# Performance work log

Measured on AMD Instinct MI355X. Metric: run time of the kernel, lower is better.

Reference implementation:

```python
import jax, jax.numpy as jnp
import numpy as np

N_NODES = 50000

def _sage_conv(x, src, dst, W_l, b_l, W_r):
    # PyG SAGEConv, aggr='mean': out = lin_l(mean_j x_j) + lin_r(x_i)
    msg = x[src]                                                 # [E, d] gather
    agg = jax.ops.segment_sum(msg, dst, num_segments=N_NODES)   # [N, d] scatter-add
    cnt = jax.ops.segment_sum(jnp.ones((src.shape[0], 1), x.dtype), dst,
                              num_segments=N_NODES)              # [N, 1] in-degree
    agg = agg / jnp.maximum(cnt, 1.0)                            # mean (0 for isolated nodes)
    return agg @ W_l + b_l + x @ W_r

def setup_inputs() -> dict:
    key = jax.random.key(0)
    ks = jax.random.split(key, 8)
    in_f, hid, out_f = 128, 128, 64
    E = 640000
    x = jax.random.normal(ks[0], (N_NODES, in_f), dtype=jnp.float32)
    edge_index = jax.random.randint(ks[1], (2, E), 0, N_NODES, dtype=jnp.int64)
    def glorot(k, fan_in, fan_out):
        lim = (6.0 / (fan_in + fan_out)) ** 0.5
        return jax.random.uniform(k, (fan_in, fan_out), jnp.float32, -lim, lim)
    return {
        "x": x,
        "edge_index": edge_index,
        "W1_l": glorot(ks[2], in_f, hid),
        "b1": jnp.zeros((hid,), jnp.float32),
        "W1_r": glorot(ks[3], in_f, hid),
        "W2_l": glorot(ks[4], hid, out_f),
        "b2": jnp.zeros((out_f,), jnp.float32),
        "W2_r": glorot(ks[5], hid, out_f),
    }

def reference(x, edge_index, W1_l, b1, W1_r, W2_l, b2, W2_r):
    src, dst = edge_index[0], edge_index[1]
    h = _sage_conv(x, src, dst, W1_l, b1, W1_r)
    h = jax.nn.relu(h)
    # dropout: eval mode -> identity (deterministic reference)
    h = _sage_conv(h, src, dst, W2_l, b2, W2_r)
    return h
```

## Files before the change

### kernel.cpp

```cpp
#include <hip/hip_runtime.h>
#include <cstddef>

static constexpr int N_NODES = 50000;
static constexpr int E_EDGES = 640000;
static constexpr int F = 128;
static constexpr int MAXD = 64;
static constexpr int NBINS = 196;
static constexpr int BINCAP = 4096;
static constexpr int EBLK  = 250;

typedef __bf16 b8 __attribute__((ext_vector_type(8)));
typedef float  f4 __attribute__((ext_vector_type(4)));
typedef float  f2 __attribute__((ext_vector_type(2)));

__device__ inline unsigned short f2bf(float f) {
    unsigned u = __float_as_uint(f);
    u += 0x7FFF + ((u >> 16) & 1);
    return (unsigned short)(u >> 16);
}

__device__ inline void accq(float* s, uint2 u) {
    f2 p;
    p = __builtin_amdgcn_cvt_pk_f32_fp8(u.x, false); s[0] += p.x; s[1] += p.y;
    p = __builtin_amdgcn_cvt_pk_f32_fp8(u.x, true);  s[2] += p.x; s[3] += p.y;
    p = __builtin_amdgcn_cvt_pk_f32_fp8(u.y, false); s[4] += p.x; s[5] += p.y;
    p = __builtin_amdgcn_cvt_pk_f32_fp8(u.y, true);  s[6] += p.x; s[7] += p.y;
}

template<int BN>
__device__ inline void pack_w_body(int t, const float* __restrict__ Wl,
                                   const float* __restrict__ Wr, uint4* __restrict__ Bp) {
    constexpr int NTg = BN / 16;
    int wid = t >> 6, lane = t & 63;
    if (wid >= 8 * NTg) return;
    int kq = lane >> 4, m = lane & 15;
    int kt = wid / NTg, nt = wid % NTg;
    unsigned short tmp[8];
#pragma unroll
    for (int j = 0; j < 8; ++j) {
        int k = kt * 32 + kq * 8 + j;
        const float* W = (k < 128) ? Wl : Wr;
        tmp[j] = f2bf(W[(size_t)(k & 127) * BN + nt * 16 + m]);
    }
    uint4 u;
    u.x = tmp[0] | ((unsigned)tmp[1] << 16);
    u.y = tmp[2] | ((unsigned)tmp[3] << 16);
    u.z = tmp[4] | ((unsigned)tmp[5] << 16);
    u.w = tmp[6] | ((unsigned)tmp[7] << 16);
    Bp[wid * 64 + lane] = u;
}

__global__ __launch_bounds__(256)
void prep(const int* __restrict__ ei, int* __restrict__ gbin, unsigned* __restrict__ binbuf,
          const float* __restrict__ x, uint4* __restrict__ xb, uint2* __restrict__ xq,
          const float* __restrict__ W1l, const float* __restrict__ W1r, uint4* __restrict__ Bp1,
          const float* __restrict__ W2l, const float* __restrict__ W2r, uint4* __restrict__ Bp2) {
    int b = blockIdx.x, tid = threadIdx.x;
    if (b < EBLK) {
        __shared__ int cnt[NBINS];
        __shared__ int base[NBINS];
        for (int i = tid; i < NBINS; i += 256) cnt[i] = 0;
        __syncthreads();
        int e0 = b * 2560;
        unsigned rec[10]; int bin[10]; int rnk[10];
#pragma unroll
        for (int k = 0; k < 10; ++k) {
            int e = e0 + k * 256 + tid;
            int s = ei[e], d = ei[E_EDGES + e];
            bin[k] = d >> 8;
            rec[k] = ((unsigned)(d & 255) << 16) | (unsigned)s;
            rnk[k] = atomicAdd(&cnt[bin[k]], 1);
        }
        __syncthreads();
        for (int i = tid; i < NBINS; i += 256)
            base[i] = atomicAdd(&gbin[i], cnt[i]);
        __syncthreads();
#pragma unroll
        for (int k = 0; k < 10; ++k) {
            int pos = base[bin[k]] + rnk[k];
            if (pos < BINCAP) binbuf[(size_t)bin[k] * BINCAP + pos] = rec[k];
        }
    } else {
        int o = b - EBLK;
        if (o < 3125) {
            int i = o * 256 + tid;
            const float4* s = (const float4*)x + (size_t)i * 2;
            float4 v0 = s[0], v1 = s[1];
            uint4 u;
            u.x = f2bf(v0.x) | ((unsigned)f2bf(v0.y) << 16);
            u.y = f2bf(v0.z) | ((unsigned)f2bf(v0.w) << 16);
            u.z = f2bf(v1.x) | ((unsigned)f2bf(v1.y) << 16);
            u.w = f2bf(v1.z) | ((unsigned)f2bf(v1.w) << 16);
            xb[i] = u;
            uint2 q;
            q.x = __builtin_amdgcn_cvt_pk_fp8_f32(v0.x, v0.y, 0, false);
            q.x = __builtin_amdgcn_cvt_pk_fp8_f32(v0.z, v0.w, q.x, true);
            q.y = __builtin_amdgcn_cvt_pk_fp8_f32(v1.x, v1.y, 0, false);
            q.y = __builtin_amdgcn_cvt_pk_fp8_f32(v1.z, v1.w, q.y, true);
            xq[i] = q;
        } else if (o < 3141) {
            pack_w_body<128>((o - 3125) * 256 + tid, W1l, W1r, Bp1);
        } else {
            pack_w_body<64>((o - 3141) * 256 + tid, W2l, W2r, Bp2);
        }
    }
}

__global__ __launch_bounds__(256)
void bucket(const unsigned* __restrict__ binbuf, const int* __restrict__ gbin,
            int* __restrict__ deg, int* __restrict__ col) {
    int b = blockIdx.x, tid = threadIdx.x;
    __shared__ int lc[256];
    lc[tid] = 0;
    __syncthreads();
    int cnt = gbin[b]; cnt = cnt < BINCAP ? cnt : BINCAP;
    const unsigned* bb = binbuf + (size_t)b * BINCAP;
    for (int i = tid; i < cnt; i += 256) {
        unsigned rec = bb[i];
        int dl = (rec >> 16) & 255;
        int s  = (int)(rec & 0xFFFFu);
        int r  = atomicAdd(&lc[dl], 1);
        if (r < MAXD) col[(((size_t)(b << 8) + dl) << 6) + r] = s;
    }
    __syncthreads();
    int node = (b << 8) + tid;
    if (node < N_NODES) deg[node] = lc[tid];
}

__global__ __launch_bounds__(256)
void sage_l1(const uint2* __restrict__ featq,
             const unsigned short* __restrict__ featb,
             const int* __restrict__ deg,
             const int* __restrict__ col,
             const unsigned short* __restrict__ Bp1,
             const unsigned short* __restrict__ Bp2,
             const float* __restrict__ b1,
             const float* __restrict__ b2,
             unsigned char* __restrict__ Zq,
             float* __restrict__ out) {
    constexpr int LDW = 68;
    __shared__ unsigned Alds[16 * LDW];
    __shared__ unsigned short Hlds[16 * 136];

    const int tid  = threadIdx.x;
    const int wv   = tid >> 6;
    const int lane = tid & 63;
    const int c    = lane & 15;
    const int g    = lane >> 4;
    const int node0 = blockIdx.x * 16;
    const int node  = node0 + wv * 4 + g;

    {
        int d0 = deg[node];
        int d  = d0 < MAXD ? d0 : MAXD;
        int jb = node << 6, je = jb + d;
        float s0[8] = {0.f,0.f,0.f,0.f,0.f,0.f,0.f,0.f};
        float s1[8] = {0.f,0.f,0.f,0.f,0.f,0.f,0.f,0.f};
        float s2[8] = {0.f,0.f,0.f,0.f,0.f,0.f,0.f,0.f};
        float s3[8] = {0.f,0.f,0.f,0.f,0.f,0.f,0.f,0.f};
        int j = jb;
        for (; j + 7 < je; j += 8) {
            uint2 u0 = featq[(size_t)col[j + 0] * 16 + c];
            uint2 u1 = featq[(size_t)col[j + 1] * 16 + c];
            uint2 u2 = featq[(size_t)col[j + 2] * 16 + c];
            uint2 u3 = featq[(size_t)col[j + 3] * 16 + c];
            uint2 u4 = featq[(size_t)col[j + 4] * 16 + c];
            uint2 u5 = featq[(size_t)col[j + 5] * 16 + c];
            uint2 u6 = featq[(size_t)col[j + 6] * 16 + c];
            uint2 u7 = featq[(size_t)col[j + 7] * 16 + c];
            accq(s0, u0); accq(s1, u1); accq(s2, u2); accq(s3, u3);
            accq(s0, u4); accq(s1, u5); accq(s2, u6); accq(s3, u7);
        }
        if (j + 3 < je) {
            uint2 u0 = featq[(size_t)col[j + 0] * 16 + c];
            uint2 u1 = featq[(size_t)col[j + 1] * 16 + c];
            uint2 u2 = featq[(size_t)col[j + 2] * 16 + c];
            uint2 u3 = featq[(size_t)col[j + 3] * 16 + c];
            accq(s0, u0); accq(s1, u1); accq(s2, u2); accq(s3, u3);
            j += 4;
        }
        for (; j < je; ++j) {
            uint2 u0 = featq[(size_t)col[j] * 16 + c];
            accq(s0, u0);
        }
        float inv = 1.0f / (float)(d > 0 ? d : 1);
        float r[8];
#pragma unroll
        for (int k = 0; k < 8; ++k) r[k] = ((s0[k] + s1[k]) + (s2[k] + s3[k])) * inv;
        uint4 o;
        o.x = f2bf(r[0]) | ((unsigned)f2bf(r[1]) << 16);
        o.y = f2bf(r[2]) | ((unsigned)f2bf(r[3]) << 16);
        o.z = f2bf(r[4]) | ((unsigned)f2bf(r[5]) << 16);
        o.w = f2bf(r[6]) | ((unsigned)f2bf(r[7]) << 16);
        *((uint4*)&Alds[(wv * 4 + g) * LDW + c * 4]) = o;
    }
    __syncthreads();

    const int m  = lane & 15;
    const int kq = lane >> 4;
    const unsigned short* srow = featb + (size_t)(node0 + m) * F + kq * 8;

    f4 zero = {0.f, 0.f, 0.f, 0.f};
    f4 acc[2] = {zero, zero};
#pragma unroll
    for (int kt = 0; kt < 8; ++kt) {
        b8 a;
        if (kt < 4) a = *((const b8*)((const char*)Alds + m * 272 + kt * 64 + kq * 16));
        else        a = *((const b8*)(srow + (kt - 4) * 32));
#pragma unroll
        for (int t = 0; t < 2; ++t) {
            int nt = wv * 2 + t;
            b8 b = *((const b8*)(Bp1 + ((size_t)(kt * 8 + nt) * 64 + lane) * 8));
            acc[t] = __builtin_amdgcn_mfma_f32_16x16x32_bf16(a, b, acc[t], 0, 0, 0);
        }
    }
    {
        int rowb = kq * 4;
#pragma unroll
        for (int t = 0; t < 2; ++t) {
            int cc = (wv * 2 + t) * 16 + m;
            float bv = b1[cc];
#pragma unroll
            for (int r = 0; r < 4; ++r) {
                float v = fmaxf(acc[t][r] + bv, 0.0f);
                Hlds[(rowb + r) * 136 + cc] = f2bf(v);
            }
        }
    }
    __syncthreads();

    f4 accZ = zero, accS = zero;
#pragma unroll
    for (int kt = 0; kt < 4; ++kt) {
        b8 a = *((const b8*)((const char*)Hlds + m * 272 + kt * 64 + kq * 16));
        b8 bz = *((const b8*)(Bp2 + ((size_t)(kt * 4 + wv) * 64 + lane) * 8));
        b8 bs = *((const b8*)(Bp2 + ((size_t)((kt + 4) * 4 + wv) * 64 + lane) * 8));
        accZ = __builtin_amdgcn_mfma_f32_16x16x32_bf16(a, bz, accZ, 0, 0, 0);
        accS = __builtin_amdgcn_mfma_f32_16x16x32_bf16(a, bs, accS, 0, 0, 0);
    }
    {
        int rowg = node0 + kq * 4;
        int cc = wv * 16 + m;
        float bv = b2[cc];
#pragma unroll
        for (int r = 0; r < 4; ++r) {
            unsigned q = __builtin_amdgcn_cvt_pk_fp8_f32(accZ[r], accZ[r], 0, false);
            Zq[(size_t)(rowg + r) * 64 + cc] = (unsigned char)(q & 0xFF);
            out[(size_t)(rowg + r) * 64 + cc] = accS[r] + bv;
        }
    }
}

__global__ __launch_bounds__(256)
void gather_add(const uint2* __restrict__ Zq,
                const int* __restrict__ deg,
                const int* __restrict__ col,
                float* __restrict__ out, int N) {
    int t = blockIdx.x * 256 + threadIdx.x;
    int node = t >> 3;
    if (node >= N) return;
    int c = t & 7;

    int d0 = deg[node];
    int d  = d0 < MAXD ? d0 : MAXD;
    int jb = node << 6, je = jb + d;
    float s0[8] = {0.f,0.f,0.f,0.f,0.f,0.f,0.f,0.f};
    float s1[8] = {0.f,0.f,0.f,0.f,0.f,0.f,0.f,0.f};
    float s2[8] = {0.f,0.f,0.f,0.f,0.f,0.f,0.f,0.f};
    float s3[8] = {0.f,0.f,0.f,0.f,0.f,0.f,0.f,0.f};
    int j = jb;
    for (; j + 7 < je; j += 8) {
        uint2 u0 = Zq[(size_t)col[j + 0] * 8 + c];
        uint2 u1 = Zq[(size_t)col[j + 1] * 8 + c];
        uint2 u2 = Zq[(size_t)col[j + 2] * 8 + c];
        uint2 u3 = Zq[(size_t)col[j + 3] * 8 + c];
        uint2 u4 = Zq[(size_t)col[j + 4] * 8 + c];
        uint2 u5 = Zq[(size_t)col[j + 5] * 8 + c];
        uint2 u6 = Zq[(size_t)col[j + 6] * 8 + c];
        uint2 u7 = Zq[(size_t)col[j + 7] * 8 + c];
        accq(s0, u0); accq(s1, u1); accq(s2, u2); accq(s3, u3);
        accq(s0, u4); accq(s1, u5); accq(s2, u6); accq(s3, u7);
    }
    if (j + 3 < je) {
        uint2 u0 = Zq[(size_t)col[j + 0] * 8 + c];
        uint2 u1 = Zq[(size_t)col[j + 1] * 8 + c];
        uint2 u2 = Zq[(size_t)col[j + 2] * 8 + c];
        uint2 u3 = Zq[(size_t)col[j + 3] * 8 + c];
        accq(s0, u0); accq(s1, u1); accq(s2, u2); accq(s3, u3);
        j += 4;
    }
    for (; j < je; ++j) {
        uint2 u0 = Zq[(size_t)col[j] * 8 + c];
        accq(s0, u0);
    }
    float inv = 1.0f / (float)(d > 0 ? d : 1);
    float* op = out + (size_t)node * 64 + c * 8;
#pragma unroll
    for (int q = 0; q < 2; ++q) {
        float4 o = *((float4*)(op + q * 4));
        o.x += ((s0[q*4+0] + s1[q*4+0]) + (s2[q*4+0] + s3[q*4+0])) * inv;
        o.y += ((s0[q*4+1] + s1[q*4+1]) + (s2[q*4+1] + s3[q*4+1])) * inv;
        o.z += ((s0[q*4+2] + s1[q*4+2]) + (s2[q*4+2] + s3[q*4+2])) * inv;
        o.w += ((s0[q*4+3] + s1[q*4+3]) + (s2[q*4+3] + s3[q*4+3])) * inv;
        *((float4*)(op + q * 4)) = o;
    }
}


extern "C" void kernel_launch(void* const* d_in, const int* in_sizes, int n_in,
                              void* d_out, int out_size, void* d_ws, size_t ws_size,
                              hipStream_t stream) {
    const float* x   = (const float*)d_in[0];
    const int*   ei  = (const int*)d_in[1];
    const float* W1l = (const float*)d_in[2];
    const float* b1  = (const float*)d_in[3];
    const float* W1r = (const float*)d_in[4];
    const float* W2l = (const float*)d_in[5];
    const float* b2  = (const float*)d_in[6];
    const float* W2r = (const float*)d_in[7];
    float* out = (float*)d_out;

    unsigned* Zq    = (unsigned*)d_ws;
    unsigned* xb    = Zq + (size_t)N_NODES * 16;
    unsigned* xq    = xb + (size_t)N_NODES * 64;
    unsigned* Bp1   = xq + (size_t)N_NODES * 32;
    unsigned* Bp2   = Bp1 + 16384;
    int* col        = (int*)(Bp2 + 8192);
    int* deg        = col + (size_t)N_NODES * MAXD;
    int* gbin       = deg + N_NODES;
    unsigned* binbuf = (unsigned*)(gbin + 256);

    hipMemsetAsync(gbin, 0, 256 * sizeof(int), stream);

    prep<<<EBLK + 3149, 256, 0, stream>>>(ei, gbin, binbuf, x, (uint4*)xb, (uint2*)xq,
                                          W1l, W1r, (uint4*)Bp1, W2l, W2r, (uint4*)Bp2);

    bucket<<<NBINS, 256, 0, stream>>>(binbuf, gbin, deg, col);

    sage_l1<<<N_NODES / 16, 256, 0, stream>>>(
        (const uint2*)xq, (const unsigned short*)xb, deg, col,
        (const unsigned short*)Bp1, (const unsigned short*)Bp2,
        b1, b2, (unsigned char*)Zq, out);

    gather_add<<<(N_NODES * 8 + 255) / 256, 256, 0, stream>>>(
        (const uint2*)Zq, deg, col, out, N_NODES);
}
```

Before: 156.1 us.

## Split neighbor gathers across two lanes per node with shuffle reduction

```diff
diff --git a/kernel.cpp b/kernel.cpp
--- a/kernel.cpp
+++ b/kernel.cpp
@@ -127,7 +127,7 @@
     if (node < N_NODES) deg[node] = lc[tid];
 }
 
-__global__ __launch_bounds__(256)
+__global__ __launch_bounds__(512)
 void sage_l1(const uint2* __restrict__ featq,
              const unsigned short* __restrict__ featb,
              const int* __restrict__ deg,
@@ -145,54 +145,63 @@
     const int tid  = threadIdx.x;
     const int wv   = tid >> 6;
     const int lane = tid & 63;
-    const int c    = lane & 15;
-    const int g    = lane >> 4;
     const int node0 = blockIdx.x * 16;
-    const int node  = node0 + wv * 4 + g;
 
     {
+        const int n  = wv * 2 + (lane >> 5);
+        const int h  = (lane >> 4) & 1;
+        const int c  = lane & 15;
+        const int node = node0 + n;
         int d0 = deg[node];
         int d  = d0 < MAXD ? d0 : MAXD;
-        int jb = node << 6, je = jb + d;
+        int jb = node << 6;
+        int dh = (d + 1 - h) >> 1;
         float s0[8] = {0.f,0.f,0.f,0.f,0.f,0.f,0.f,0.f};
         float s1[8] = {0.f,0.f,0.f,0.f,0.f,0.f,0.f,0.f};
         float s2[8] = {0.f,0.f,0.f,0.f,0.f,0.f,0.f,0.f};
         float s3[8] = {0.f,0.f,0.f,0.f,0.f,0.f,0.f,0.f};
-        int j = jb;
-        for (; j + 7 < je; j += 8) {
-            uint2 u0 = featq[(size_t)col[j + 0] * 16 + c];
-            uint2 u1 = featq[(size_t)col[j + 1] * 16 + c];
-            uint2 u2 = featq[(size_t)col[j + 2] * 16 + c];
-            uint2 u3 = featq[(size_t)col[j + 3] * 16 + c];
-            uint2 u4 = featq[(size_t)col[j + 4] * 16 + c];
-            uint2 u5 = featq[(size_t)col[j + 5] * 16 + c];
-            uint2 u6 = featq[(size_t)col[j + 6] * 16 + c];
-            uint2 u7 = featq[(size_t)col[j + 7] * 16 + c];
+        int j = jb + h;
+        int rem = dh;
+        for (; rem >= 8; rem -= 8, j += 16) {
+            uint2 u0 = featq[(size_t)col[j +  0] * 16 + c];
+            uint2 u1 = featq[(size_t)col[j +  2] * 16 + c];
+            uint2 u2 = featq[(size_t)col[j +  4] * 16 + c];
+            uint2 u3 = featq[(size_t)col[j +  6] * 16 + c];
+            uint2 u4 = featq[(size_t)col[j +  8] * 16 + c];
+            uint2 u5 = featq[(size_t)col[j + 10] * 16 + c];
+            uint2 u6 = featq[(size_t)col[j + 12] * 16 + c];
+            uint2 u7 = featq[(size_t)col[j + 14] * 16 + c];
             accq(s0, u0); accq(s1, u1); accq(s2, u2); accq(s3, u3);
             accq(s0, u4); accq(s1, u5); accq(s2, u6); accq(s3, u7);
         }
-        if (j + 3 < je) {
+        if (rem >= 4) {
             uint2 u0 = featq[(size_t)col[j + 0] * 16 + c];
-            uint2 u1 = featq[(size_t)col[j + 1] * 16 + c];
-            uint2 u2 = featq[(size_t)col[j + 2] * 16 + c];
-            uint2 u3 = featq[(size_t)col[j + 3] * 16 + c];
+            uint2 u1 = featq[(size_t)col[j + 2] * 16 + c];
+            uint2 u2 = featq[(size_t)col[j + 4] * 16 + c];
+            uint2 u3 = featq[(size_t)col[j + 6] * 16 + c];
             accq(s0, u0); accq(s1, u1); accq(s2, u2); accq(s3, u3);
-            j += 4;
-        }
-        for (; j < je; ++j) {
+            rem -= 4; j += 8;
+        }
+        for (; rem > 0; --rem, j += 2) {
             uint2 u0 = featq[(size_t)col[j] * 16 + c];
             accq(s0, u0);
         }
         float inv = 1.0f / (float)(d > 0 ? d : 1);
         float r[8];
 #pragma unroll
-        for (int k = 0; k < 8; ++k) r[k] = ((s0[k] + s1[k]) + (s2[k] + s3[k])) * inv;
-        uint4 o;
-        o.x = f2bf(r[0]) | ((unsigned)f2bf(r[1]) << 16);
-        o.y = f2bf(r[2]) | ((unsigned)f2bf(r[3]) << 16);
-        o.z = f2bf(r[4]) | ((unsigned)f2bf(r[5]) << 16);
-        o.w = f2bf(r[6]) | ((unsigned)f2bf(r[7]) << 16);
-        *((uint4*)&Alds[(wv * 4 + g) * LDW + c * 4]) = o;
+        for (int k = 0; k < 8; ++k) {
+            float v = (s0[k] + s1[k]) + (s2[k] + s3[k]);
+            v += __shfl_xor(v, 16);
+            r[k] = v * inv;
+        }
+        if (h == 0) {
+            uint4 o;
+            o.x = f2bf(r[0]) | ((unsigned)f2bf(r[1]) << 16);
+            o.y = f2bf(r[2]) | ((unsigned)f2bf(r[3]) << 16);
+            o.z = f2bf(r[4]) | ((unsigned)f2bf(r[5]) << 16);
+            o.w = f2bf(r[6]) | ((unsigned)f2bf(r[7]) << 16);
+            *((uint4*)&Alds[n * LDW + c * 4]) = o;
+        }
     }
     __syncthreads();
 
@@ -201,52 +210,51 @@
     const unsigned short* srow = featb + (size_t)(node0 + m) * F + kq * 8;
 
     f4 zero = {0.f, 0.f, 0.f, 0.f};
-    f4 acc[2] = {zero, zero};
-#pragma unroll
-    for (int kt = 0; kt < 8; ++kt) {
-        b8 a;
-        if (kt < 4) a = *((const b8*)((const char*)Alds + m * 272 + kt * 64 + kq * 16));
-        else        a = *((const b8*)(srow + (kt - 4) * 32));
-#pragma unroll
-        for (int t = 0; t < 2; ++t) {
-            int nt = wv * 2 + t;
-            b8 b = *((const b8*)(Bp1 + ((size_t)(kt * 8 + nt) * 64 + lane) * 8));
-            acc[t] = __builtin_amdgcn_mfma_f32_16x16x32_bf16(a, b, acc[t], 0, 0, 0);
-        }
-    }
     {
+        f4 acc = zero;
+#pragma unroll
+        for (int kt = 0; kt < 8; ++kt) {
+            b8 a;
+            if (kt < 4) a = *((const b8*)((const char*)Alds + m * 272 + kt * 64 + kq * 16));
+            else        a = *((const b8*)(srow + (kt - 4) * 32));
+            b8 b = *((const b8*)(Bp1 + ((size_t)(kt * 8 + wv) * 64 + lane) * 8));
+            acc = __builtin_amdgcn_mfma_f32_16x16x32_bf16(a, b, acc, 0, 0, 0);
+        }
         int rowb = kq * 4;
-#pragma unroll
-        for (int t = 0; t < 2; ++t) {
-            int cc = (wv * 2 + t) * 16 + m;
-            float bv = b1[cc];
+        int cc = wv * 16 + m;
+        float bv = b1[cc];
+#pragma unroll
+        for (int r = 0; r < 4; ++r) {
+            float v = fmaxf(acc[r] + bv, 0.0f);
+            Hlds[(rowb + r) * 136 + cc] = f2bf(v);
+        }
+    }
+    __syncthreads();
+
+    {
+        const int colid = wv & 3;
+        const bool isZ = (wv < 4);
+        const int boff = isZ ? 0 : 16;
+        f4 acc = zero;
+#pragma unroll
+        for (int kt = 0; kt < 4; ++kt) {
+            b8 a = *((const b8*)((const char*)Hlds + m * 272 + kt * 64 + kq * 16));
+            b8 b = *((const b8*)(Bp2 + ((size_t)(kt * 4 + colid + boff) * 64 + lane) * 8));
+            acc = __builtin_amdgcn_mfma_f32_16x16x32_bf16(a, b, acc, 0, 0, 0);
+        }
+        int rowg = node0 + kq * 4;
+        int cc = colid * 16 + m;
+        if (isZ) {
 #pragma unroll
             for (int r = 0; r < 4; ++r) {
-                float v = fmaxf(acc[t][r] + bv, 0.0f);
-                Hlds[(rowb + r) * 136 + cc] = f2bf(v);
+                unsigned q = __builtin_amdgcn_cvt_pk_fp8_f32(acc[r], acc[r], 0, false);
+                Zq[(size_t)(rowg + r) * 64 + cc] = (unsigned char)(q & 0xFF);
             }
-        }
-    }
-    __syncthreads();
-
-    f4 accZ = zero, accS = zero;
-#pragma unroll
-    for (int kt = 0; kt < 4; ++kt) {
-        b8 a = *((const b8*)((const char*)Hlds + m * 272 + kt * 64 + kq * 16));
-        b8 bz = *((const b8*)(Bp2 + ((size_t)(kt * 4 + wv) * 64 + lane) * 8));
-        b8 bs = *((const b8*)(Bp2 + ((size_t)((kt + 4) * 4 + wv) * 64 + lane) * 8));
-        accZ = __builtin_amdgcn_mfma_f32_16x16x32_bf16(a, bz, accZ, 0, 0, 0);
-        accS = __builtin_amdgcn_mfma_f32_16x16x32_bf16(a, bs, accS, 0, 0, 0);
-    }
-    {
-        int rowg = node0 + kq * 4;
-        int cc = wv * 16 + m;
-        float bv = b2[cc];
-#pragma unroll
-        for (int r = 0; r < 4; ++r) {
-            unsigned q = __builtin_amdgcn_cvt_pk_fp8_f32(accZ[r], accZ[r], 0, false);
-            Zq[(size_t)(rowg + r) * 64 + cc] = (unsigned char)(q & 0xFF);
-            out[(size_t)(rowg + r) * 64 + cc] = accS[r] + bv;
+        } else {
+            float bv = b2[cc];
+#pragma unroll
+            for (int r = 0; r < 4; ++r)
+                out[(size_t)(rowg + r) * 64 + cc] = acc[r] + bv;
         }
     }
 }
@@ -257,52 +265,64 @@
                 const int* __restrict__ col,
                 float* __restrict__ out, int N) {
     int t = blockIdx.x * 256 + threadIdx.x;
-    int node = t >> 3;
+    int node = t >> 4;
     if (node >= N) return;
     int c = t & 7;
+    int h = (t >> 3) & 1;
 
     int d0 = deg[node];
     int d  = d0 < MAXD ? d0 : MAXD;
-    int jb = node << 6, je = jb + d;
+    int jb = node << 6;
+    int dh = (d + 1 - h) >> 1;
     float s0[8] = {0.f,0.f,0.f,0.f,0.f,0.f,0.f,0.f};
     float s1[8] = {0.f,0.f,0.f,0.f,0.f,0.f,0.f,0.f};
     float s2[8] = {0.f,0.f,0.f,0.f,0.f,0.f,0.f,0.f};
     float s3[8] = {0.f,0.f,0.f,0.f,0.f,0.f,0.f,0.f};
-    int j = jb;
-    for (; j + 7 < je; j += 8) {
-        uint2 u0 = Zq[(size_t)col[j + 0] * 8 + c];
-        uint2 u1 = Zq[(size_t)col[j + 1] * 8 + c];
-        uint2 u2 = Zq[(size_t)col[j + 2] * 8 + c];
-        uint2 u3 = Zq[(size_t)col[j + 3] * 8 + c];
-        uint2 u4 = Zq[(size_t)col[j + 4] * 8 + c];
-        uint2 u5 = Zq[(size_t)col[j + 5] * 8 + c];
-        uint2 u6 = Zq[(size_t)col[j + 6] * 8 + c];
-        uint2 u7 = Zq[(size_t)col[j + 7] * 8 + c];
+    int j = jb + h;
+    int rem = dh;
+    for (; rem >= 8; rem -= 8, j += 16) {
+        uint2 u0 = Zq[(size_t)col[j +  0] * 8 + c];
+        uint2 u1 = Zq[(size_t)col[j +  2] * 8 + c];
+        uint2 u2 = Zq[(size_t)col[j +  4] * 8 + c];
+        uint2 u3 = Zq[(size_t)col[j +  6] * 8 + c];
+        uint2 u4 = Zq[(size_t)col[j +  8] * 8 + c];
+        uint2 u5 = Zq[(size_t)col[j + 10] * 8 + c];
+        uint2 u6 = Zq[(size_t)col[j + 12] * 8 + c];
+        uint2 u7 = Zq[(size_t)col[j + 14] * 8 + c];
         accq(s0, u0); accq(s1, u1); accq(s2, u2); accq(s3, u3);
         accq(s0, u4); accq(s1, u5); accq(s2, u6); accq(s3, u7);
     }
-    if (j + 3 < je) {
+    if (rem >= 4) {
         uint2 u0 = Zq[(size_t)col[j + 0] * 8 + c];
-        uint2 u1 = Zq[(size_t)col[j + 1] * 8 + c];
-        uint2 u2 = Zq[(size_t)col[j + 2] * 8 + c];
-        uint2 u3 = Zq[(size_t)col[j + 3] * 8 + c];
+        uint2 u1 = Zq[(size_t)col[j + 2] * 8 + c];
+        uint2 u2 = Zq[(size_t)col[j + 4] * 8 + c];
+        uint2 u3 = Zq[(size_t)col[j + 6] * 8 + c];
         accq(s0, u0); accq(s1, u1); accq(s2, u2); accq(s3, u3);
-        j += 4;
-    }
-    for (; j < je; ++j) {
+        rem -= 4; j += 8;
+    }
+    for (; rem > 0; --rem, j += 2) {
         uint2 u0 = Zq[(size_t)col[j] * 8 + c];
         accq(s0, u0);
     }
     float inv = 1.0f / (float)(d > 0 ? d : 1);
-    float* op = out + (size_t)node * 64 + c * 8;
-#pragma unroll
-    for (int q = 0; q < 2; ++q) {
-        float4 o = *((float4*)(op + q * 4));
-        o.x += ((s0[q*4+0] + s1[q*4+0]) + (s2[q*4+0] + s3[q*4+0])) * inv;
-        o.y += ((s0[q*4+1] + s1[q*4+1]) + (s2[q*4+1] + s3[q*4+1])) * inv;
-        o.z += ((s0[q*4+2] + s1[q*4+2]) + (s2[q*4+2] + s3[q*4+2])) * inv;
-        o.w += ((s0[q*4+3] + s1[q*4+3]) + (s2[q*4+3] + s3[q*4+3])) * inv;
-        *((float4*)(op + q * 4)) = o;
+    float r[8];
+#pragma unroll
+    for (int k = 0; k < 8; ++k) {
+        float v = (s0[k] + s1[k]) + (s2[k] + s3[k]);
+        v += __shfl_xor(v, 8);
+        r[k] = v * inv;
+    }
+    if (h == 0) {
+        float* op = out + (size_t)node * 64 + c * 8;
+#pragma unroll
+        for (int q = 0; q < 2; ++q) {
+            float4 o = *((float4*)(op + q * 4));
+            o.x += r[q*4+0];
+            o.y += r[q*4+1];
+            o.z += r[q*4+2];
+            o.w += r[q*4+3];
+            *((float4*)(op + q * 4)) = o;
+        }
     }
 }
 
@@ -337,11 +357,11 @@
 
     bucket<<<NBINS, 256, 0, stream>>>(binbuf, gbin, deg, col);
 
-    sage_l1<<<N_NODES / 16, 256, 0, stream>>>(
+    sage_l1<<<N_NODES / 16, 512, 0, stream>>>(
         (const uint2*)xq, (const unsigned short*)xb, deg, col,
         (const unsigned short*)Bp1, (const unsigned short*)Bp2,
         b1, b2, (unsigned char*)Zq, out);
 
-    gather_add<<<(N_NODES * 8 + 255) / 256, 256, 0, stream>>>(
+    gather_add<<<(N_NODES * 16 + 255) / 256, 256, 0, stream>>>(
         (const uint2*)Zq, deg, col, out, N_NODES);
 }
```

After: 169.2 us. +8.4%, slower.
